# Kernel tuning notes

Hardware: AMD Instinct MI355X
Metric: run time of the kernel (lower is better)

The kernel has to match this reference:

```python
import jax, jax.numpy as jnp
import numpy as np

B, H, S, DK = 2, 16, 2048, 64


def setup_inputs() -> dict:
    key = jax.random.key(0)
    kq, kk, kv = jax.random.split(key, 3)
    q = jax.random.normal(kq, (B, H, S, DK), dtype=jnp.float32)
    k = jax.random.normal(kk, (B, H, S, DK), dtype=jnp.float32)
    v = jax.random.normal(kv, (B, H, S, DK), dtype=jnp.float32)
    # 3-D boolean mask [B, Sq, Sk]; True = allowed. Causal lower-triangular.
    mask = jnp.broadcast_to(jnp.tril(jnp.ones((S, S), dtype=bool)), (B, S, S))
    return {"q": q, "k": k, "v": v, "mask": mask}


def reference(q, k, v, mask):
    # scores: [B, H, Sq, Sk]
    scores = jnp.einsum("bhqd,bhkd->bhqk", q, k) / jnp.sqrt(jnp.asarray(DK, q.dtype))
    if mask.ndim == scores.ndim - 1:
        mask = mask[:, None, :, :]  # broadcast over heads
    scores = jnp.where(mask, scores, jnp.asarray(-jnp.inf, scores.dtype))
    attn = jax.nn.softmax(scores, axis=-1)
    out = jnp.einsum("bhqk,bhkd->bhqd", attn, v)
    return out
```

## Files before the change

### kernel.cpp

```cpp
#include <hip/hip_runtime.h>


typedef float    v4f __attribute__((ext_vector_type(4)));
typedef _Float16 v4h __attribute__((ext_vector_type(4)));
typedef _Float16 v8h __attribute__((ext_vector_type(8)));

#define SEQ 2048
#define DKC 64

#if __has_builtin(__builtin_amdgcn_exp2f)
#define EXP2(x) __builtin_amdgcn_exp2f(x)
#else
#define EXP2(x) exp2f(x)
#endif

#define MFMA16(a,b,c) __builtin_amdgcn_mfma_f32_16x16x16f16(a,b,c,0,0,0)
#define MFMA32(a,b,c) __builtin_amdgcn_mfma_f32_16x16x32_f16(a,b,c,0,0,0)

__global__ __launch_bounds__(256) void prep_kv(const float* __restrict__ k,
                                               const float* __restrict__ v,
                                               _Float16* __restrict__ kh,
                                               _Float16* __restrict__ vt) {
  const int bh = blockIdx.x;
  const int kt = blockIdx.y;
  const int tid = threadIdx.x;
  {
    const int quad = tid & 3;
    const int l16  = (tid >> 2) & 15;
    const int st   = (tid >> 6) & 1;
    const int s    = tid >> 7;
    const float* src = k + ((size_t)bh * SEQ + kt * 32 + s * 16 + l16) * DKC + st * 32 + quad * 8;
    float4 a = *(const float4*)src;
    float4 b = *(const float4*)(src + 4);
    v8h h;
    h[0] = (_Float16)a.x; h[1] = (_Float16)a.y; h[2] = (_Float16)a.z; h[3] = (_Float16)a.w;
    h[4] = (_Float16)b.x; h[5] = (_Float16)b.y; h[6] = (_Float16)b.z; h[7] = (_Float16)b.w;
    *(v8h*)(kh + (size_t)bh * SEQ * DKC
               + (size_t)(kt * 4 + s * 2 + st) * 512 + (quad * 16 + l16) * 8) = h;
  }
  {
    const int d = tid & 63, q4 = tid >> 6;
    const float* src = v + ((size_t)bh * SEQ + kt * 32) * DKC + d;
    v8h h;
#pragma unroll
    for (int j = 0; j < 4; ++j) h[j]     = (_Float16)src[(size_t)(q4 * 4 + j) * DKC];
#pragma unroll
    for (int j = 0; j < 4; ++j) h[4 + j] = (_Float16)src[(size_t)(16 + q4 * 4 + j) * DKC];
    *(v8h*)(vt + (size_t)bh * SEQ * DKC + (size_t)kt * 2048
               + (d >> 4) * 512 + (q4 * 16 + (d & 15)) * 8) = h;
  }
}

__device__ __forceinline__ void compute_chunk(int k0, bool straddle, int qw, int l16, int quad,
                                              const v8h (&qf)[2][2],
                                              const v8h (&kf)[4], const v8h (&va)[4],
                                              v4f (&O)[2][4], v4f (&L)[2], const v4h ones) {
  v4f S[2][2] = {};
#pragma unroll
  for (int t = 0; t < 2; ++t)
#pragma unroll
    for (int s = 0; s < 2; ++s) {
      S[t][s] = MFMA32(kf[s * 2 + 0], qf[t][0], S[t][s]);
      S[t][s] = MFMA32(kf[s * 2 + 1], qf[t][1], S[t][s]);
    }

  if (straddle) {
#pragma unroll
    for (int t = 0; t < 2; ++t) {
      const int qg = qw + t * 16 + l16;
#pragma unroll
      for (int s = 0; s < 2; ++s) {
        const int kb = k0 + s * 16 + quad * 4;
#pragma unroll
        for (int r = 0; r < 4; ++r)
          if (kb + r > qg) S[t][s][r] = -3e38f;
      }
    }
  }

  v4h pf[2][2];
#pragma unroll
  for (int t = 0; t < 2; ++t)
#pragma unroll
    for (int s = 0; s < 2; ++s) {
      v4h p;
#pragma unroll
      for (int r = 0; r < 4; ++r) p[r] = (_Float16)EXP2(S[t][s][r]);
      pf[t][s] = p;
    }

#pragma unroll
  for (int dc = 0; dc < 4; ++dc) {
    v4h lo = __builtin_shufflevector(va[dc], va[dc], 0, 1, 2, 3);
    v4h hi = __builtin_shufflevector(va[dc], va[dc], 4, 5, 6, 7);
    O[0][dc] = MFMA16(lo, pf[0][0], O[0][dc]);
    O[0][dc] = MFMA16(hi, pf[0][1], O[0][dc]);
    O[1][dc] = MFMA16(lo, pf[1][0], O[1][dc]);
    O[1][dc] = MFMA16(hi, pf[1][1], O[1][dc]);
  }
  L[0] = MFMA16(ones, pf[0][0], L[0]);
  L[0] = MFMA16(ones, pf[0][1], L[0]);
  L[1] = MFMA16(ones, pf[1][0], L[1]);
  L[1] = MFMA16(ones, pf[1][1], L[1]);
}

#define GLD16(gp, lp) __builtin_amdgcn_global_load_lds(                     \
    (const __attribute__((address_space(1))) void*)(gp),                    \
    (__attribute__((address_space(3))) void*)(lp), 16, 0, 0)

#define STAGE(bf, c) do {                                                   \
    const char* _gk = khb + (size_t)(c) * 16384 + wv * 1024 + lane * 16;    \
    const char* _gv = vtb + (size_t)(c) * 16384 + wv * 1024 + lane * 16;    \
    char* _lk = ((char*)&lds[bf][0][0]) + wv * 1024;                        \
    char* _lv = ((char*)&lds[bf][1][0]) + wv * 1024;                        \
    GLD16(_gk, _lk);                                                        \
    GLD16(_gv, _lv);                                                        \
  } while (0)

__global__ __launch_bounds__(1024, 4) void fa_fwd(const float* __restrict__ q,
                                                  const _Float16* __restrict__ kh,
                                                  const _Float16* __restrict__ vt,
                                                  float* __restrict__ out) {
  __shared__ __align__(16) char smem[122880];
  _Float16 (*lds)[2][8192] = reinterpret_cast<_Float16(*)[2][8192]>(smem);
  v4f (*cb)[4][10][64]     = reinterpret_cast<v4f(*)[4][10][64]>(smem);

  const int lane = threadIdx.x & 63;
  const int wv   = threadIdx.x >> 6;
  const int w    = wv & 3;
  const int grp  = wv >> 2;
  const int quad = lane >> 4;
  const int l16  = lane & 15;

  const int g  = (int)blockIdx.x & 7;
  const int r  = (int)blockIdx.x >> 3;
  const int bh = g * 4 + (r & 3);
  const int p  = r >> 2;

  const size_t base = (size_t)bh * SEQ * DKC;
  const char* khb = (const char*)(kh + base);
  const char* vtb = (const char*)(vt + base);

  const float CSC = 0.18033688011112042f;
  const v4h ones = {(_Float16)1.f, (_Float16)1.f, (_Float16)1.f, (_Float16)1.f};

  for (int ph = 0; ph < 2; ++ph) {
    const int qb  = ph ? (15 - p) : p;
    const int qw  = qb * 128 + w * 32;
    const int myk = qb * 4 + w;
    const int NC  = qb + 1;

    v8h qf[2][2];
#pragma unroll
    for (int t = 0; t < 2; ++t)
#pragma unroll
      for (int st = 0; st < 2; ++st) {
        const float* qr = q + base + (size_t)(qw + t * 16 + l16) * DKC + st * 32 + quad * 8;
        float4 a = *(const float4*)qr;
        float4 b = *(const float4*)(qr + 4);
        v8h hq;
        hq[0] = (_Float16)(a.x * CSC); hq[1] = (_Float16)(a.y * CSC);
        hq[2] = (_Float16)(a.z * CSC); hq[3] = (_Float16)(a.w * CSC);
        hq[4] = (_Float16)(b.x * CSC); hq[5] = (_Float16)(b.y * CSC);
        hq[6] = (_Float16)(b.z * CSC); hq[7] = (_Float16)(b.w * CSC);
        qf[t][st] = hq;
      }

    v4f O[2][4] = {};
    v4f L[2]    = {};

    STAGE(0, 0);
    __syncthreads();

    for (int c = 0; c < NC; ++c) {
      if (c + 1 < NC) STAGE((c + 1) & 1, c + 1);
      const int b = c & 1;
      const int kt32 = c * 4 + grp;
      if (kt32 <= myk) {
        v8h kf[4], va[4];
#pragma unroll
        for (int i = 0; i < 4; ++i) kf[i] = *(const v8h*)&lds[b][0][grp * 2048 + i * 512 + lane * 8];
#pragma unroll
        for (int i = 0; i < 4; ++i) va[i] = *(const v8h*)&lds[b][1][grp * 2048 + i * 512 + lane * 8];
        compute_chunk(kt32 * 32, kt32 == myk, qw, l16, quad, qf, kf, va, O, L, ones);
      }
      __syncthreads();
    }

    const int red = ph;
    if (grp != red) {
      const int s = (grp < red) ? grp : grp - 1;
#pragma unroll
      for (int t = 0; t < 2; ++t) {
#pragma unroll
        for (int dc = 0; dc < 4; ++dc) cb[s][w][t * 4 + dc][lane] = O[t][dc];
        cb[s][w][8 + t][lane] = L[t];
      }
    }
    __syncthreads();
    if (grp == red) {
#pragma unroll
      for (int s = 0; s < 3; ++s)
#pragma unroll
        for (int t = 0; t < 2; ++t) {
#pragma unroll
          for (int dc = 0; dc < 4; ++dc) O[t][dc] += cb[s][w][t * 4 + dc][lane];
          L[t] += cb[s][w][8 + t][lane];
        }
#pragma unroll
      for (int t = 0; t < 2; ++t) {
        const float inv = 1.0f / L[t][0];
        float* orow = out + base + (size_t)(qw + t * 16 + l16) * DKC + quad * 4;
#pragma unroll
        for (int dc = 0; dc < 4; ++dc) {
          float4 o;
          o.x = O[t][dc][0] * inv; o.y = O[t][dc][1] * inv;
          o.z = O[t][dc][2] * inv; o.w = O[t][dc][3] * inv;
          *(float4*)(orow + dc * 16) = o;
        }
      }
    }
    __syncthreads();
  }
}

extern "C" void kernel_launch(void* const* d_in, const int* in_sizes, int n_in,
                              void* d_out, int out_size, void* d_ws, size_t ws_size,
                              hipStream_t stream) {
  (void)in_sizes; (void)n_in; (void)out_size; (void)ws_size;
  const float* q = (const float*)d_in[0];
  const float* k = (const float*)d_in[1];
  const float* v = (const float*)d_in[2];
  float* out = (float*)d_out;

  _Float16* kh = (_Float16*)d_ws;
  _Float16* vt = (_Float16*)((char*)d_ws + (size_t)32 * SEQ * DKC * 2);

  prep_kv<<<dim3(32, 64), dim3(256), 0, stream>>>(k, v, kh, vt);
  fa_fwd<<<dim3(256), dim3(1024), 0, stream>>>(q, kh, vt, out);
}
```

Measured before the change: 136.3 us.

## Deepen K/V LDS pipeline to four buffers and process two chunks per barrier

Grows the shared-memory ring from two to four K/V chunk buffers. The loop now prefetches two chunks ahead and computes two chunks between each block-wide barrier, where before it prefetched one chunk and synchronised after every chunk. The aim is to hide more global-to-LDS latency and halve the number of __syncthreads calls. The cost is more LDS per block, which may be tight on a CU that holds one 1024-thread block, and more in-flight loads.

```diff
diff --git a/kernel.cpp b/kernel.cpp
--- a/kernel.cpp
+++ b/kernel.cpp
@@ -117,11 +117,26 @@
     GLD16(_gv, _lv);                                                        \
   } while (0)
 
+#define UNIT(cc) do {                                                       \
+    const int _b = (cc) & 3;                                                \
+    const int _kt32 = (cc) * 4 + grp;                                       \
+    if (_kt32 <= myk) {                                                     \
+      v8h kf[4], va[4];                                                     \
+      _Pragma("unroll")                                                     \
+      for (int i = 0; i < 4; ++i)                                           \
+        kf[i] = *(const v8h*)&lds[_b][0][grp * 2048 + i * 512 + lane * 8];  \
+      _Pragma("unroll")                                                     \
+      for (int i = 0; i < 4; ++i)                                           \
+        va[i] = *(const v8h*)&lds[_b][1][grp * 2048 + i * 512 + lane * 8];  \
+      compute_chunk(_kt32 * 32, _kt32 == myk, qw, l16, quad, qf, kf, va, O, L, ones); \
+    }                                                                       \
+  } while (0)
+
 __global__ __launch_bounds__(1024, 4) void fa_fwd(const float* __restrict__ q,
                                                   const _Float16* __restrict__ kh,
                                                   const _Float16* __restrict__ vt,
                                                   float* __restrict__ out) {
-  __shared__ __align__(16) char smem[122880];
+  __shared__ __align__(16) char smem[131072];
   _Float16 (*lds)[2][8192] = reinterpret_cast<_Float16(*)[2][8192]>(smem);
   v4f (*cb)[4][10][64]     = reinterpret_cast<v4f(*)[4][10][64]>(smem);
 
@@ -170,20 +185,14 @@
     v4f L[2]    = {};
 
     STAGE(0, 0);
+    if (NC > 1) STAGE(1, 1);
     __syncthreads();
 
-    for (int c = 0; c < NC; ++c) {
-      if (c + 1 < NC) STAGE((c + 1) & 1, c + 1);
-      const int b = c & 1;
-      const int kt32 = c * 4 + grp;
-      if (kt32 <= myk) {
-        v8h kf[4], va[4];
-#pragma unroll
-        for (int i = 0; i < 4; ++i) kf[i] = *(const v8h*)&lds[b][0][grp * 2048 + i * 512 + lane * 8];
-#pragma unroll
-        for (int i = 0; i < 4; ++i) va[i] = *(const v8h*)&lds[b][1][grp * 2048 + i * 512 + lane * 8];
-        compute_chunk(kt32 * 32, kt32 == myk, qw, l16, quad, qf, kf, va, O, L, ones);
-      }
+    for (int c = 0; c < NC; c += 2) {
+      if (c + 2 < NC) STAGE((c + 2) & 3, c + 2);
+      if (c + 3 < NC) STAGE((c + 3) & 3, c + 3);
+      UNIT(c);
+      if (c + 1 < NC) UNIT(c + 1);
       __syncthreads();
     }
 
```

Measured after the change: 139.8 us. 1.03x slower.
